# Kernel optimization log

Hardware: AMD Instinct MI355X
Metric: run time of the kernel (lower is better)

## Reference

```python
import math
import jax, jax.numpy as jnp
import numpy as np

N_HEADS = 16
LOCAL_HEADS = 8
GLOBAL_HEADS = N_HEADS - LOCAL_HEADS
WINDOW = 256
NEG_INF = -1e30


def setup_inputs() -> dict:
    key = jax.random.key(0)
    ks = jax.random.split(key, 6)
    B, S, E = 1, 4096, 1024
    inp = {
        "hidden_states": jax.random.normal(ks[0], (B, S, E), dtype=jnp.float32),
        "Wq": jax.random.normal(ks[1], (E, E), dtype=jnp.float32) * (1.0 / math.sqrt(E)),
        "Wk": jax.random.normal(ks[2], (E, E), dtype=jnp.float32) * (1.0 / math.sqrt(E)),
        "Wv": jax.random.normal(ks[3], (E, E), dtype=jnp.float32) * (1.0 / math.sqrt(E)),
        "Wo": jax.random.normal(ks[4], (E, E), dtype=jnp.float32) * (1.0 / math.sqrt(E)),
        "bo": jnp.zeros((E,), dtype=jnp.float32),
    }
    return inp


def reference(hidden_states, Wq, Wk, Wv, Wo, bo):
    B, S, E = hidden_states.shape
    H, D = N_HEADS, E // N_HEADS
    scale = 1.0 / math.sqrt(D)

    def proj(W):
        # nn.Linear: x @ W.T ; reshape to [B, H, S, D]
        y = jnp.einsum('bse,fe->bsf', hidden_states, W)
        return y.reshape(B, S, H, D).transpose(0, 2, 1, 3)

    q = proj(Wq) * scale
    k = proj(Wk)
    v = proj(Wv)

    i = jnp.arange(S)[:, None]
    j = jnp.arange(S)[None, :]
    causal = j <= i                      # [S, S] allowed positions
    local = causal & (j >= i - WINDOW)   # sliding window of width WINDOW+1

    def attend(qh, kh, vh, mask):
        scores = jnp.einsum('bhsd,bhtd->bhst', qh, kh)
        scores = jnp.where(mask, scores, NEG_INF)
        w = jax.nn.softmax(scores, axis=-1)
        return jnp.einsum('bhst,bhtd->bhsd', w, vh)

    out_g = attend(q[:, :GLOBAL_HEADS], k[:, :GLOBAL_HEADS], v[:, :GLOBAL_HEADS], causal)
    out_l = attend(q[:, GLOBAL_HEADS:], k[:, GLOBAL_HEADS:], v[:, GLOBAL_HEADS:], local)

    attn = jnp.concatenate([out_g, out_l], axis=1)       # [B, H, S, D]
    attn = attn.transpose(0, 2, 1, 3).reshape(B, S, E)    # [B, S, E]
    return jnp.einsum('bse,fe->bsf', attn, Wo) + bo
```

## Files before the change

### kernel.cpp

```cpp
#include <hip/hip_runtime.h>
#include <hip/hip_fp16.h>

#define S_LEN 4096
#define EMB   1024
#define NH    16
#define HD    64
#define GH    8
#define WIN   256

typedef _Float16 half8 __attribute__((ext_vector_type(8)));
typedef float    f32x4 __attribute__((ext_vector_type(4)));
typedef unsigned short ushort8 __attribute__((ext_vector_type(8)));

static __device__ __forceinline__ f32x4 mfma16(half8 a, half8 b, f32x4 c) {
    return __builtin_amdgcn_mfma_f32_16x16x32_f16(a, b, c, 0, 0, 0);
}

#define GLOAD16(g, l) __builtin_amdgcn_global_load_lds( \
    (const __attribute__((address_space(1))) void*)(g), \
    (__attribute__((address_space(3))) void*)(l), 16, 0, 0)

__global__ __launch_bounds__(256) void split_kernel(
    const float* __restrict__ X,  const float* __restrict__ Wq, const float* __restrict__ Wk,
    const float* __restrict__ Wv, const float* __restrict__ Wo,
    __half* __restrict__ Xhi, __half* __restrict__ Xlo,
    __half* __restrict__ Wh,  __half* __restrict__ Wl,
    __half* __restrict__ Woh, __half* __restrict__ Wol)
{
    const int NT = gridDim.x * blockDim.x;
    for (int i = blockIdx.x * blockDim.x + threadIdx.x; i < 2097152; i += NT) {
        const float* src; __half *dh, *dl; int off;
        if (i < 1048576)      { src = X;  dh = Xhi;           dl = Xlo;           off = i; }
        else if (i < 1310720) { src = Wq; dh = Wh;            dl = Wl;            off = i - 1048576; }
        else if (i < 1572864) { src = Wk; dh = Wh + 1048576;  dl = Wl + 1048576;  off = i - 1310720; }
        else if (i < 1835008) { src = Wv; dh = Wh + 2097152;  dl = Wl + 2097152;  off = i - 1572864; }
        else                  { src = Wo; dh = Woh;           dl = Wol;           off = i - 1835008; }
        float4 xv = *(const float4*)(src + (size_t)off * 4);
        union { __half h[4]; uint2 u; } ph, pl;
        float xs[4] = {xv.x, xv.y, xv.z, xv.w};
        #pragma unroll
        for (int j = 0; j < 4; ++j) {
            __half hj = __float2half_rn(xs[j]);
            ph.h[j] = hj;
            pl.h[j] = __float2half_rn(xs[j] - __half2float(hj));
        }
        *(uint2*)(dh + (size_t)off * 4) = ph.u;
        *(uint2*)(dl + (size_t)off * 4) = pl.u;
    }
}

__global__ __launch_bounds__(256) void gemm_split_kernel(
    const __half* __restrict__ Ah_, const __half* __restrict__ Al_,
    const __half* __restrict__ Bh_, const __half* __restrict__ Bl_,
    int mode, __half* __restrict__ qkv_out,
    float* __restrict__ fo_out, const float* __restrict__ bias)
{
    __shared__ __align__(16) char lds[65536];
    char* LA_h = lds;
    char* LA_l = lds + 16384;
    char* LB_h = lds + 32768;
    char* LB_l = lds + 49152;

    const int tid  = threadIdx.x;
    const int w    = tid >> 6, lane = tid & 63;
    const int bm   = blockIdx.x * 128, bn = blockIdx.y * 128;
    const int wm0  = (w & 1) * 64, wn0 = (w >> 1) * 64;
    const int lr   = lane & 15;
    const int lk   = lane >> 4;

    const char *gAh[4], *gAl[4], *gBh[4], *gBl[4];
    int ldsoff[4];
    #pragma unroll
    for (int i = 0; i < 4; ++i) {
        const int c = tid + i * 256;
        const int row = c >> 3;
        const int sw  = ((c & 7) ^ (row & 7)) * 16;
        gAh[i] = (const char*)Ah_ + (size_t)(bm + row) * 2048 + sw;
        gAl[i] = (const char*)Al_ + (size_t)(bm + row) * 2048 + sw;
        gBh[i] = (const char*)Bh_ + (size_t)(bn + row) * 2048 + sw;
        gBl[i] = (const char*)Bl_ + (size_t)(bn + row) * 2048 + sw;
        ldsoff[i] = ((tid >> 6) * 64 + i * 256) * 16;
    }

    f32x4 acc[4][4];
    #pragma unroll
    for (int mi = 0; mi < 4; ++mi)
        #pragma unroll
        for (int ni = 0; ni < 4; ++ni) acc[mi][ni] = (f32x4){0.f, 0.f, 0.f, 0.f};

    for (int k0 = 0; k0 < 1024; k0 += 64) {
        __syncthreads();
        const size_t kb = (size_t)k0 * 2;
        #pragma unroll
        for (int i = 0; i < 4; ++i) {
            GLOAD16(gAh[i] + kb, LA_h + ldsoff[i]);
            GLOAD16(gAl[i] + kb, LA_l + ldsoff[i]);
            GLOAD16(gBh[i] + kb, LB_h + ldsoff[i]);
            GLOAD16(gBl[i] + kb, LB_l + ldsoff[i]);
        }
        __syncthreads();

        #pragma unroll
        for (int kh = 0; kh < 2; ++kh) {
            half8 afh[4], afl[4], bfh[4], bfl[4];
            #pragma unroll
            for (int f = 0; f < 4; ++f) {
                const int ar = wm0 + f * 16 + lr;
                const int ab = ar * 128 + ((kh * 64 + lk * 16) ^ ((ar & 7) << 4));
                afh[f] = *(const half8*)(LA_h + ab);
                afl[f] = *(const half8*)(LA_l + ab);
                const int br = wn0 + f * 16 + lr;
                const int bb = br * 128 + ((kh * 64 + lk * 16) ^ ((br & 7) << 4));
                bfh[f] = *(const half8*)(LB_h + bb);
                bfl[f] = *(const half8*)(LB_l + bb);
            }
            #pragma unroll
            for (int mi = 0; mi < 4; ++mi)
                #pragma unroll
                for (int ni = 0; ni < 4; ++ni) {
                    acc[mi][ni] = mfma16(afh[mi], bfh[ni], acc[mi][ni]);
                    acc[mi][ni] = mfma16(afh[mi], bfl[ni], acc[mi][ni]);
                    acc[mi][ni] = mfma16(afl[mi], bfh[ni], acc[mi][ni]);
                }
        }
    }

    if (mode == 0) {
        #pragma unroll
        for (int ni = 0; ni < 4; ++ni) {
            const int n  = bn + wn0 + ni * 16 + lr;
            const int hg = n >> 6;
            const int d  = n & 63;
            const float alpha = ((n >> 10) == 0) ? 0.125f : 1.0f;
            __half* base = qkv_out + (size_t)hg * S_LEN * HD + d;
            #pragma unroll
            for (int mi = 0; mi < 4; ++mi) {
                const int m = bm + wm0 + mi * 16 + lk * 4;
                #pragma unroll
                for (int r = 0; r < 4; ++r)
                    base[(size_t)(m + r) * HD] = __float2half_rn(acc[mi][ni][r] * alpha);
            }
        }
    } else {
        #pragma unroll
        for (int ni = 0; ni < 4; ++ni) {
            const int n = bn + wn0 + ni * 16 + lr;
            const float bv = bias[n];
            #pragma unroll
            for (int mi = 0; mi < 4; ++mi) {
                const int m = bm + wm0 + mi * 16 + lk * 4;
                #pragma unroll
                for (int r = 0; r < 4; ++r)
                    fo_out[(size_t)(m + r) * EMB + n] = acc[mi][ni][r] + bv;
            }
        }
    }
}

__global__ __launch_bounds__(256) void attn_pass1(
    const __half* __restrict__ q, const __half* __restrict__ k, const __half* __restrict__ v,
    __half* __restrict__ Ohi, __half* __restrict__ Olo,
    float* __restrict__ partO, float* __restrict__ partML)
{
    __shared__ __align__(16) unsigned char smem[32768];
    char* Qs = (char*)smem;
    char* Ks = (char*)smem + 8192;
    char* Vt = (char*)smem + 16384;
    char* Pl = (char*)smem + 24576;

    int h, qb, kt_lo, kt_hi, pslot = 0;
    bool is_local, direct;
    if (blockIdx.x < 160) {
        h = blockIdx.y;
        is_local = false;
        const int i = 159 - blockIdx.x;
        int c;
        if (i < 16)      { qb = i;                c = 0; }
        else if (i < 48) { const int t = i - 16;  qb = 16 + (t >> 1); c = t & 1; }
        else if (i < 96) { const int t = i - 48;  qb = 32 + t / 3;    c = t % 3; }
        else             { const int t = i - 96;  qb = 48 + (t >> 2); c = t & 3; }
        kt_lo = c * 16;
        kt_hi = (kt_lo + 15 < qb) ? kt_lo + 15 : qb;
        direct = (qb < 16);
        pslot  = (h * 48 + (qb - 16)) * 4 + c;
    } else {
        h  = 8 + blockIdx.y;
        qb = blockIdx.x - 160;
        is_local = true;
        kt_lo = (qb - 4 > 0) ? qb - 4 : 0;
        kt_hi = qb;
        direct = true;
    }

    const int tid  = threadIdx.x;
    const int w    = tid >> 6;
    const int lane = tid & 63;
    const int lq   = lane & 15;
    const int hi   = lane >> 4;

    const char* qh = (const char*)(q + (size_t)h * S_LEN * HD);
    const char* kh = (const char*)(k + (size_t)h * S_LEN * HD);
    const char* vh = (const char*)(v + (size_t)h * S_LEN * HD);

    #pragma unroll
    for (int e = 0; e < 2; ++e) {
        const int flat = e * 4096 + tid * 16;
        const int row  = flat >> 7;
        const int src  = flat ^ ((row & 7) << 4);
        *(uint4*)(Qs + flat) = *(const uint4*)(qh + (size_t)qb * 8192 + src);
    }
    __syncthreads();

    half8 qf[2];
    #pragma unroll
    for (int ks = 0; ks < 2; ++ks) {
        const int row = w * 16 + lq;
        int byte = row * 128 + hi * 16 + ks * 64;
        byte ^= (row & 7) << 4;
        qf[ks] = *(const half8*)(Qs + byte);
    }

    float m_run = -1e30f, l_run = 0.f;
    f32x4 po[4];
    #pragma unroll
    for (int i = 0; i < 4; ++i) po[i] = (f32x4){0.f, 0.f, 0.f, 0.f};

    const int qg = qb * 64 + w * 16 + lq;
    char* plw = Pl + w * 2048;

    for (int kv = kt_lo; kv <= kt_hi; ++kv) {
        __syncthreads();

        #pragma unroll
        for (int e = 0; e < 2; ++e) {
            const int flat = e * 4096 + tid * 16;
            const int row  = flat >> 7;
            const int src  = flat ^ ((row & 7) << 4);
            *(uint4*)(Ks + flat) = *(const uint4*)(kh + (size_t)kv * 8192 + src);
        }
        {
            const int j0 = (tid & 31) * 2;
            const int d0 = (tid >> 5) * 8;
            ushort8 v0 = *(const ushort8*)(vh + (size_t)(kv * 64 + j0)     * 128 + d0 * 2);
            ushort8 v1 = *(const ushort8*)(vh + (size_t)(kv * 64 + j0 + 1) * 128 + d0 * 2);
            #pragma unroll
            for (int i = 0; i < 8; ++i) {
                const int d = d0 + i;
                int byte = d * 128 + j0 * 2;
                byte ^= (d & 7) << 4;
                *(unsigned int*)(Vt + byte) = (unsigned int)v0[i] | ((unsigned int)v1[i] << 16);
            }
        }
        __syncthreads();

        f32x4 st[4];
        #pragma unroll
        for (int i = 0; i < 4; ++i) st[i] = (f32x4){0.f, 0.f, 0.f, 0.f};
        #pragma unroll
        for (int ks = 0; ks < 2; ++ks) {
            #pragma unroll
            for (int kt = 0; kt < 4; ++kt) {
                const int row = kt * 16 + lq;
                int byte = row * 128 + hi * 16 + ks * 64;
                byte ^= (row & 7) << 4;
                half8 kf = *(const half8*)(Ks + byte);
                st[kt] = mfma16(kf, qf[ks], st[kt]);
            }
        }

        float mx = -1e30f;
        #pragma unroll
        for (int kt = 0; kt < 4; ++kt)
            #pragma unroll
            for (int r = 0; r < 4; ++r) {
                const int kg = kv * 64 + kt * 16 + hi * 4 + r;
                const bool ok = (kg <= qg) && (!is_local || (kg + WIN >= qg));
                const float s = ok ? st[kt][r] : -1e30f;
                st[kt][r] = s;
                mx = fmaxf(mx, s);
            }
        mx = fmaxf(mx, __shfl_xor(mx, 16));
        mx = fmaxf(mx, __shfl_xor(mx, 32));
        const float mnew  = fmaxf(m_run, mx);
        const float scale = __expf(m_run - mnew);
        float lsum = 0.f;
        #pragma unroll
        for (int kt = 0; kt < 4; ++kt)
            #pragma unroll
            for (int r = 0; r < 4; ++r) {
                const float p = __expf(st[kt][r] - mnew);
                st[kt][r] = p;
                lsum += p;
            }
        lsum += __shfl_xor(lsum, 16);
        lsum += __shfl_xor(lsum, 32);
        l_run = l_run * scale + lsum;
        m_run = mnew;
        #pragma unroll
        for (int dt = 0; dt < 4; ++dt)
            #pragma unroll
            for (int r = 0; r < 4; ++r) po[dt][r] *= scale;

        #pragma unroll
        for (int kt = 0; kt < 4; ++kt) {
            int byte = lq * 128 + kt * 32 + hi * 8;
            byte ^= (lq & 7) << 4;
            union { __half2 h2[2]; uint2 u; } pu;
            pu.h2[0] = __floats2half2_rn(st[kt][0], st[kt][1]);
            pu.h2[1] = __floats2half2_rn(st[kt][2], st[kt][3]);
            *(uint2*)(plw + byte) = pu.u;
        }

        #pragma unroll
        for (int ks = 0; ks < 2; ++ks) {
            int pbyte = lq * 128 + ks * 64 + hi * 16;
            pbyte ^= (lq & 7) << 4;
            half8 pf = *(const half8*)(plw + pbyte);
            #pragma unroll
            for (int dt = 0; dt < 4; ++dt) {
                const int drow = dt * 16 + lq;
                int vbyte = drow * 128 + ks * 64 + hi * 16;
                vbyte ^= (drow & 7) << 4;
                half8 vf = *(const half8*)(Vt + vbyte);
                po[dt] = mfma16(vf, pf, po[dt]);
            }
        }
    }

    if (direct) {
        const float linv = 1.0f / l_run;
        __half* oh = Ohi + (size_t)qg * EMB + h * HD;
        __half* ol = Olo + (size_t)qg * EMB + h * HD;
        #pragma unroll
        for (int dt = 0; dt < 4; ++dt)
            #pragma unroll
            for (int r = 0; r < 4; ++r) {
                const float vfull = po[dt][r] * linv;
                const __half vhi = __float2half_rn(vfull);
                oh[dt * 16 + hi * 4 + r] = vhi;
                ol[dt * 16 + hi * 4 + r] = __float2half_rn(vfull - __half2float(vhi));
            }
    } else {
        float* op = partO + (size_t)pslot * 4096 + (w * 16 + lq) * 64;
        #pragma unroll
        for (int dt = 0; dt < 4; ++dt)
            #pragma unroll
            for (int r = 0; r < 4; ++r)
                op[dt * 16 + hi * 4 + r] = po[dt][r];
        if (hi == 0) {
            partML[(size_t)pslot * 128 + (w * 16 + lq) * 2]     = m_run;
            partML[(size_t)pslot * 128 + (w * 16 + lq) * 2 + 1] = l_run;
        }
    }
}

__global__ __launch_bounds__(256) void attn_combine(
    const float* __restrict__ partO, const float* __restrict__ partML,
    __half* __restrict__ Ohi, __half* __restrict__ Olo)
{
    const int qb = 16 + blockIdx.x;
    const int h  = blockIdx.y;
    const int nc = (qb >> 4) + 1;
    const int row = threadIdx.x >> 2;
    const int d0  = (threadIdx.x & 3) * 16;
    const int base_slot = (h * 48 + (qb - 16)) * 4;

    float M = -1e30f, mv[4], lv[4];
    #pragma unroll
    for (int i = 0; i < 4; ++i)
        if (i < nc) {
            mv[i] = partML[(size_t)(base_slot + i) * 128 + row * 2];
            lv[i] = partML[(size_t)(base_slot + i) * 128 + row * 2 + 1];
            M = fmaxf(M, mv[i]);
        }
    float L = 0.f, wgt[4];
    #pragma unroll
    for (int i = 0; i < 4; ++i)
        if (i < nc) {
            wgt[i] = __expf(mv[i] - M);
            L += lv[i] * wgt[i];
        }

    float o[16];
    #pragma unroll
    for (int j = 0; j < 16; ++j) o[j] = 0.f;
    #pragma unroll
    for (int i = 0; i < 4; ++i)
        if (i < nc) {
            const float* src = partO + (size_t)(base_slot + i) * 4096 + row * 64 + d0;
            const float wi = wgt[i];
            #pragma unroll
            for (int j4 = 0; j4 < 4; ++j4) {
                float4 s4 = *(const float4*)(src + j4 * 4);
                o[j4*4+0] = fmaf(wi, s4.x, o[j4*4+0]);
                o[j4*4+1] = fmaf(wi, s4.y, o[j4*4+1]);
                o[j4*4+2] = fmaf(wi, s4.z, o[j4*4+2]);
                o[j4*4+3] = fmaf(wi, s4.w, o[j4*4+3]);
            }
        }
    const float Linv = 1.0f / L;
    ushort8 ph[2], pl[2];
    #pragma unroll
    for (int j = 0; j < 16; ++j) {
        const float vfull = o[j] * Linv;
        const __half vhi = __float2half_rn(vfull);
        ph[j >> 3][j & 7] = __half_as_ushort(vhi);
        pl[j >> 3][j & 7] = __half_as_ushort(__float2half_rn(vfull - __half2float(vhi)));
    }
    const size_t ob = (size_t)(qb * 64 + row) * EMB + h * HD + d0;
    *(ushort8*)((__half*)Ohi + ob)     = ph[0];
    *(ushort8*)((__half*)Ohi + ob + 8) = ph[1];
    *(ushort8*)((__half*)Olo + ob)     = pl[0];
    *(ushort8*)((__half*)Olo + ob + 8) = pl[1];
}

extern "C" void kernel_launch(void* const* d_in, const int* in_sizes, int n_in,
                              void* d_out, int out_size, void* d_ws, size_t ws_size,
                              hipStream_t stream) {
    const float* X  = (const float*)d_in[0];
    const float* Wq = (const float*)d_in[1];
    const float* Wk = (const float*)d_in[2];
    const float* Wv = (const float*)d_in[3];
    const float* Wo = (const float*)d_in[4];
    const float* bo = (const float*)d_in[5];
    float* out = (float*)d_out;

    __half* ws   = (__half*)d_ws;
    __half* qkvb = ws;
    __half* XOhi = ws + 12582912;
    __half* XOlo = ws + 16777216;
    __half* Woh  = ws + 20971520;
    __half* Wol  = ws + 22020096;
    __half* Wh   = ws + 23068672;
    __half* Wl   = ws + 26214400;
    float* partO  = (float*)(ws + 23068672);
    float* partML = partO + 6291456;

    split_kernel<<<dim3(2048), 256, 0, stream>>>(X, Wq, Wk, Wv, Wo,
                                                 XOhi, XOlo, Wh, Wl, Woh, Wol);
    gemm_split_kernel<<<dim3(32, 24), 256, 0, stream>>>(XOhi, XOlo, Wh, Wl,
                                                        0, qkvb, nullptr, nullptr);
    attn_pass1<<<dim3(224, 8), 256, 0, stream>>>(qkvb, qkvb + 4194304, qkvb + 8388608,
                                                 XOhi, XOlo, partO, partML);
    attn_combine<<<dim3(48, 8), 256, 0, stream>>>(partO, partML, XOhi, XOlo);
    gemm_split_kernel<<<dim3(32, 8), 256, 0, stream>>>(XOhi, XOlo, Woh, Wol,
                                                       1, nullptr, out, bo);
}
```

Baseline: 262.9 us.

## Use plain fp16 for output projection instead of split hi/lo emulation

The attention output and Wo are now stored only as fp16 hi parts, and a new dedicated fp16 GEMM kernel with 128x64 tiles computes the output projection using one MFMA per tile step instead of three. Attention and combine kernels stop writing the low-order residual, and the split kernel skips Wo's low part. This cuts MFMA work and memory traffic for the final GEMM at the cost of reduced accuracy in the output projection.

```diff
diff --git a/kernel.cpp b/kernel.cpp
--- a/kernel.cpp
+++ b/kernel.cpp
@@ -25,7 +25,7 @@
     const float* __restrict__ Wv, const float* __restrict__ Wo,
     __half* __restrict__ Xhi, __half* __restrict__ Xlo,
     __half* __restrict__ Wh,  __half* __restrict__ Wl,
-    __half* __restrict__ Woh, __half* __restrict__ Wol)
+    __half* __restrict__ Woh)
 {
     const int NT = gridDim.x * blockDim.x;
     for (int i = blockIdx.x * blockDim.x + threadIdx.x; i < 2097152; i += NT) {
@@ -34,7 +34,7 @@
         else if (i < 1310720) { src = Wq; dh = Wh;            dl = Wl;            off = i - 1048576; }
         else if (i < 1572864) { src = Wk; dh = Wh + 1048576;  dl = Wl + 1048576;  off = i - 1310720; }
         else if (i < 1835008) { src = Wv; dh = Wh + 2097152;  dl = Wl + 2097152;  off = i - 1572864; }
-        else                  { src = Wo; dh = Woh;           dl = Wol;           off = i - 1835008; }
+        else                  { src = Wo; dh = Woh;           dl = nullptr;       off = i - 1835008; }
         float4 xv = *(const float4*)(src + (size_t)off * 4);
         union { __half h[4]; uint2 u; } ph, pl;
         float xs[4] = {xv.x, xv.y, xv.z, xv.w};
@@ -45,15 +45,14 @@
             pl.h[j] = __float2half_rn(xs[j] - __half2float(hj));
         }
         *(uint2*)(dh + (size_t)off * 4) = ph.u;
-        *(uint2*)(dl + (size_t)off * 4) = pl.u;
+        if (dl) *(uint2*)(dl + (size_t)off * 4) = pl.u;
     }
 }
 
 __global__ __launch_bounds__(256) void gemm_split_kernel(
     const __half* __restrict__ Ah_, const __half* __restrict__ Al_,
     const __half* __restrict__ Bh_, const __half* __restrict__ Bl_,
-    int mode, __half* __restrict__ qkv_out,
-    float* __restrict__ fo_out, const float* __restrict__ bias)
+    __half* __restrict__ qkv_out)
 {
     __shared__ __align__(16) char lds[65536];
     char* LA_h = lds;
@@ -125,41 +124,110 @@
         }
     }
 
-    if (mode == 0) {
-        #pragma unroll
-        for (int ni = 0; ni < 4; ++ni) {
-            const int n  = bn + wn0 + ni * 16 + lr;
-            const int hg = n >> 6;
-            const int d  = n & 63;
-            const float alpha = ((n >> 10) == 0) ? 0.125f : 1.0f;
-            __half* base = qkv_out + (size_t)hg * S_LEN * HD + d;
-            #pragma unroll
-            for (int mi = 0; mi < 4; ++mi) {
-                const int m = bm + wm0 + mi * 16 + lk * 4;
+    #pragma unroll
+    for (int ni = 0; ni < 4; ++ni) {
+        const int n  = bn + wn0 + ni * 16 + lr;
+        const int hg = n >> 6;
+        const int d  = n & 63;
+        const float alpha = ((n >> 10) == 0) ? 0.125f : 1.0f;
+        __half* base = qkv_out + (size_t)hg * S_LEN * HD + d;
+        #pragma unroll
+        for (int mi = 0; mi < 4; ++mi) {
+            const int m = bm + wm0 + mi * 16 + lk * 4;
+            #pragma unroll
+            for (int r = 0; r < 4; ++r)
+                base[(size_t)(m + r) * HD] = __float2half_rn(acc[mi][ni][r] * alpha);
+        }
+    }
+}
+
+__global__ __launch_bounds__(256) void gemm_out_f16_kernel(
+    const __half* __restrict__ A_, const __half* __restrict__ B_,
+    float* __restrict__ fo_out, const float* __restrict__ bias)
+{
+    __shared__ __align__(16) char lds[24576];
+    char* LA = lds;
+    char* LB = lds + 16384;
+
+    const int tid  = threadIdx.x;
+    const int w    = tid >> 6, lane = tid & 63;
+    const int bm   = blockIdx.x * 128, bn = blockIdx.y * 64;
+    const int wm0  = (w & 1) * 64, wn0 = (w >> 1) * 32;
+    const int lr   = lane & 15;
+    const int lk   = lane >> 4;
+
+    const char *gA[4], *gB[2];
+    int loA[4], loB[2];
+    #pragma unroll
+    for (int i = 0; i < 4; ++i) {
+        const int c = tid + i * 256;
+        const int row = c >> 3;
+        const int sw  = ((c & 7) ^ (row & 7)) * 16;
+        gA[i] = (const char*)A_ + (size_t)(bm + row) * 2048 + sw;
+        loA[i] = (w * 64 + i * 256) * 16;
+    }
+    #pragma unroll
+    for (int i = 0; i < 2; ++i) {
+        const int c = tid + i * 256;
+        const int row = c >> 3;
+        const int sw  = ((c & 7) ^ (row & 7)) * 16;
+        gB[i] = (const char*)B_ + (size_t)(bn + row) * 2048 + sw;
+        loB[i] = (w * 64 + i * 256) * 16;
+    }
+
+    f32x4 acc[4][2];
+    #pragma unroll
+    for (int mi = 0; mi < 4; ++mi)
+        #pragma unroll
+        for (int ni = 0; ni < 2; ++ni) acc[mi][ni] = (f32x4){0.f, 0.f, 0.f, 0.f};
+
+    for (int k0 = 0; k0 < 1024; k0 += 64) {
+        __syncthreads();
+        const size_t kb = (size_t)k0 * 2;
+        #pragma unroll
+        for (int i = 0; i < 4; ++i) GLOAD16(gA[i] + kb, LA + loA[i]);
+        #pragma unroll
+        for (int i = 0; i < 2; ++i) GLOAD16(gB[i] + kb, LB + loB[i]);
+        __syncthreads();
+
+        #pragma unroll
+        for (int kh = 0; kh < 2; ++kh) {
+            half8 af[4], bf[2];
+            #pragma unroll
+            for (int f = 0; f < 4; ++f) {
+                const int ar = wm0 + f * 16 + lr;
+                af[f] = *(const half8*)(LA + ar * 128 + ((kh * 64 + lk * 16) ^ ((ar & 7) << 4)));
+            }
+            #pragma unroll
+            for (int ni = 0; ni < 2; ++ni) {
+                const int br = wn0 + ni * 16 + lr;
+                bf[ni] = *(const half8*)(LB + br * 128 + ((kh * 64 + lk * 16) ^ ((br & 7) << 4)));
+            }
+            #pragma unroll
+            for (int mi = 0; mi < 4; ++mi)
                 #pragma unroll
-                for (int r = 0; r < 4; ++r)
-                    base[(size_t)(m + r) * HD] = __float2half_rn(acc[mi][ni][r] * alpha);
-            }
-        }
-    } else {
-        #pragma unroll
-        for (int ni = 0; ni < 4; ++ni) {
-            const int n = bn + wn0 + ni * 16 + lr;
-            const float bv = bias[n];
-            #pragma unroll
-            for (int mi = 0; mi < 4; ++mi) {
-                const int m = bm + wm0 + mi * 16 + lk * 4;
-                #pragma unroll
-                for (int r = 0; r < 4; ++r)
-                    fo_out[(size_t)(m + r) * EMB + n] = acc[mi][ni][r] + bv;
-            }
+                for (int ni = 0; ni < 2; ++ni)
+                    acc[mi][ni] = mfma16(af[mi], bf[ni], acc[mi][ni]);
+        }
+    }
+
+    #pragma unroll
+    for (int ni = 0; ni < 2; ++ni) {
+        const int n = bn + wn0 + ni * 16 + lr;
+        const float bv = bias[n];
+        #pragma unroll
+        for (int mi = 0; mi < 4; ++mi) {
+            const int m = bm + wm0 + mi * 16 + lk * 4;
+            #pragma unroll
+            for (int r = 0; r < 4; ++r)
+                fo_out[(size_t)(m + r) * EMB + n] = acc[mi][ni][r] + bv;
         }
     }
 }
 
 __global__ __launch_bounds__(256) void attn_pass1(
     const __half* __restrict__ q, const __half* __restrict__ k, const __half* __restrict__ v,
-    __half* __restrict__ Ohi, __half* __restrict__ Olo,
+    __half* __restrict__ Oh,
     float* __restrict__ partO, float* __restrict__ partML)
 {
     __shared__ __align__(16) unsigned char smem[32768];
@@ -329,17 +397,12 @@
 
     if (direct) {
         const float linv = 1.0f / l_run;
-        __half* oh = Ohi + (size_t)qg * EMB + h * HD;
-        __half* ol = Olo + (size_t)qg * EMB + h * HD;
+        __half* oh = Oh + (size_t)qg * EMB + h * HD;
         #pragma unroll
         for (int dt = 0; dt < 4; ++dt)
             #pragma unroll
-            for (int r = 0; r < 4; ++r) {
-                const float vfull = po[dt][r] * linv;
-                const __half vhi = __float2half_rn(vfull);
-                oh[dt * 16 + hi * 4 + r] = vhi;
-                ol[dt * 16 + hi * 4 + r] = __float2half_rn(vfull - __half2float(vhi));
-            }
+            for (int r = 0; r < 4; ++r)
+                oh[dt * 16 + hi * 4 + r] = __float2half_rn(po[dt][r] * linv);
     } else {
         float* op = partO + (size_t)pslot * 4096 + (w * 16 + lq) * 64;
         #pragma unroll
@@ -356,7 +419,7 @@
 
 __global__ __launch_bounds__(256) void attn_combine(
     const float* __restrict__ partO, const float* __restrict__ partML,
-    __half* __restrict__ Ohi, __half* __restrict__ Olo)
+    __half* __restrict__ Oh)
 {
     const int qb = 16 + blockIdx.x;
     const int h  = blockIdx.y;
@@ -399,19 +462,13 @@
             }
         }
     const float Linv = 1.0f / L;
-    ushort8 ph[2], pl[2];
-    #pragma unroll
-    for (int j = 0; j < 16; ++j) {
-        const float vfull = o[j] * Linv;
-        const __half vhi = __float2half_rn(vfull);
-        ph[j >> 3][j & 7] = __half_as_ushort(vhi);
-        pl[j >> 3][j & 7] = __half_as_ushort(__float2half_rn(vfull - __half2float(vhi)));
-    }
+    ushort8 ph[2];
+    #pragma unroll
+    for (int j = 0; j < 16; ++j)
+        ph[j >> 3][j & 7] = __half_as_ushort(__float2half_rn(o[j] * Linv));
     const size_t ob = (size_t)(qb * 64 + row) * EMB + h * HD + d0;
-    *(ushort8*)((__half*)Ohi + ob)     = ph[0];
-    *(ushort8*)((__half*)Ohi + ob + 8) = ph[1];
-    *(ushort8*)((__half*)Olo + ob)     = pl[0];
-    *(ushort8*)((__half*)Olo + ob + 8) = pl[1];
+    *(ushort8*)((__half*)Oh + ob)     = ph[0];
+    *(ushort8*)((__half*)Oh + ob + 8) = ph[1];
 }
 
 extern "C" void kernel_launch(void* const* d_in, const int* in_sizes, int n_in,
@@ -430,19 +487,16 @@
     __half* XOhi = ws + 12582912;
     __half* XOlo = ws + 16777216;
     __half* Woh  = ws + 20971520;
-    __half* Wol  = ws + 22020096;
     __half* Wh   = ws + 23068672;
     __half* Wl   = ws + 26214400;
     float* partO  = (float*)(ws + 23068672);
     float* partML = partO + 6291456;
 
     split_kernel<<<dim3(2048), 256, 0, stream>>>(X, Wq, Wk, Wv, Wo,
-                                                 XOhi, XOlo, Wh, Wl, Woh, Wol);
-    gemm_split_kernel<<<dim3(32, 24), 256, 0, stream>>>(XOhi, XOlo, Wh, Wl,
-                                                        0, qkvb, nullptr, nullptr);
+                                                 XOhi, XOlo, Wh, Wl, Woh);
+    gemm_split_kernel<<<dim3(32, 24), 256, 0, stream>>>(XOhi, XOlo, Wh, Wl, qkvb);
     attn_pass1<<<dim3(224, 8), 256, 0, stream>>>(qkvb, qkvb + 4194304, qkvb + 8388608,
-                                                 XOhi, XOlo, partO, partML);
-    attn_combine<<<dim3(48, 8), 256, 0, stream>>>(partO, partML, XOhi, XOlo);
-    gemm_split_kernel<<<dim3(32, 8), 256, 0, stream>>>(XOhi, XOlo, Woh, Wol,
-                                                       1, nullptr, out, bo);
-}
+                                                 XOhi, partO, partML);
+    attn_combine<<<dim3(48, 8), 256, 0, stream>>>(partO, partML, XOhi);
+    gemm_out_f16_kernel<<<dim3(32, 16), 256, 0, stream>>>(XOhi, Woh, out, bo);
+}
```

Measured after the change: 252.9 us. -3.8%, faster.
